# Optimization experiments

Measured on AMD Instinct MI355X. Metric: run time of the kernel, lower is better.

Reference implementation:

```python
import jax, jax.numpy as jnp
import numpy as np

D_MODEL = 1024
NUM_HEADS = 16
D_FF = 4096
EPS = 1e-6


def _layernorm(x, alpha, beta):
    # custom LN: alpha * (x - mean) / (std + eps) + beta, std is UNBIASED (ddof=1)
    mu = jnp.mean(x, axis=-1, keepdims=True)
    var = jnp.sum((x - mu) ** 2, axis=-1, keepdims=True) / (x.shape[-1] - 1)
    return alpha * (x - mu) / (jnp.sqrt(var) + EPS) + beta


def setup_inputs() -> dict:
    key = jax.random.key(0)
    ks = jax.random.split(key, 8)
    B, S, D, F = 1, 4096, D_MODEL, D_FF
    s = 0.02
    inp = {
        "x": jax.random.normal(ks[0], (B, S, D), dtype=jnp.float32),
        "Wq": jax.random.normal(ks[1], (D, D), dtype=jnp.float32) * s,
        "bq": jnp.zeros((D,), jnp.float32),
        "Wk": jax.random.normal(ks[2], (D, D), dtype=jnp.float32) * s,
        "bk": jnp.zeros((D,), jnp.float32),
        "Wv": jax.random.normal(ks[3], (D, D), dtype=jnp.float32) * s,
        "bv": jnp.zeros((D,), jnp.float32),
        "Wo": jax.random.normal(ks[4], (D, D), dtype=jnp.float32) * s,
        "bo": jnp.zeros((D,), jnp.float32),
        "ln1_a": jnp.ones((1,), jnp.float32),
        "ln1_b": jnp.zeros((1,), jnp.float32),
        "W1": jax.random.normal(ks[5], (D, F), dtype=jnp.float32) * s,
        "b1": jnp.zeros((F,), jnp.float32),
        "W2": jax.random.normal(ks[6], (F, D), dtype=jnp.float32) * s,
        "b2": jnp.zeros((D,), jnp.float32),
        "ln2_a": jnp.ones((1,), jnp.float32),
        "ln2_b": jnp.zeros((1,), jnp.float32),
    }
    return inp


def reference(x, Wq, bq, Wk, bk, Wv, bv, Wo, bo, ln1_a, ln1_b,
              W1, b1, W2, b2, ln2_a, ln2_b):
    B, S, D = x.shape
    H = NUM_HEADS
    dk = D // H

    # --- residual 1: pre-LN self-attention ---
    h = _layernorm(x, ln1_a, ln1_b)
    Q = (h @ Wq + bq).reshape(B, S, H, dk)
    K = (h @ Wk + bk).reshape(B, S, H, dk)
    V = (h @ Wv + bv).reshape(B, S, H, dk)
    scores = jnp.einsum("bqhd,bkhd->bhqk", Q, K) / jnp.sqrt(jnp.float32(dk))
    attn = jax.nn.softmax(scores, axis=-1)  # [B,H,S,S] materialized as in source
    ctx = jnp.einsum("bhqk,bkhd->bqhd", attn, V).reshape(B, S, D)
    x = x + (ctx @ Wo + bo)  # dropout=0 -> identity

    # --- residual 2: pre-LN feed-forward ---
    h2 = _layernorm(x, ln2_a, ln2_b)
    ffn = jax.nn.relu(h2 @ W1 + b1) @ W2 + b2
    return x + ffn
```

## Files before the change

kernel.cpp:

```cpp
#include <hip/hip_runtime.h>
#include <hip/hip_bf16.h>

typedef __attribute__((ext_vector_type(8))) __bf16 bf16x8;
typedef __attribute__((ext_vector_type(4))) float f32x4;
typedef __attribute__((ext_vector_type(4))) short sh4;
typedef __attribute__((ext_vector_type(8))) short sh8;

#define MFMA(a, b, c) __builtin_amdgcn_mfma_f32_16x16x32_bf16(a, b, c, 0, 0, 0)

#if __has_builtin(__builtin_amdgcn_exp2f)
#define EXP2(x) __builtin_amdgcn_exp2f(x)
#else
#define EXP2(x) exp2f(x)
#endif

union P8 { struct { sh4 lo, hi; } p; sh8 v; };

__device__ __forceinline__ sh4 pk4(float a, float b, float c, float d) {
    __hip_bfloat162 lo = __float22bfloat162_rn(float2{a, b});
    __hip_bfloat162 hi = __float22bfloat162_rn(float2{c, d});
    union { struct { __hip_bfloat162 lo, hi; } p; sh4 s; } u;
    u.p.lo = lo; u.p.hi = hi;
    return u.s;
}

__device__ __forceinline__ float ldany(const void* p, size_t i, bool f32) {
    return f32 ? ((const float*)p)[i] : (float)(((const __bf16*)p)[i]);
}

__global__ void prep_k(const void* wq, float* flag,
                       const void* bq, const void* bk, const void* bv, const void* bo,
                       const void* b1, const void* b2,
                       const void* l1a, const void* l1b, const void* l2a, const void* l2b,
                       __bf16* dst) {
    __shared__ float red[256];
    __shared__ float fls;
    int tid = threadIdx.x;
    const __bf16* p = (const __bf16*)wq;
    float mx = 0.f;
    for (int i = tid; i < 1024; i += 256) {
        float v = (float)p[i];
        if (v != v) mx = 2.f;
        v = fabsf(v);
        if (v > mx) mx = v;
    }
    red[tid] = mx;
    __syncthreads();
    for (int s = 128; s > 0; s >>= 1) {
        if (tid < s) red[tid] = fmaxf(red[tid], red[tid + s]);
        __syncthreads();
    }
    if (tid == 0) { fls = (red[0] > 1.0f) ? 1.f : 0.f; *flag = fls; }
    __syncthreads();
    bool f32 = fls > 0.5f;
    const void* srcs[10] = {bq, bk, bv, bo, b1, b2, l1a, l1b, l2a, l2b};
    const int offs[10] = {1024, 2048, 3072, 4096, 5120, 9216, 10240, 10241, 10242, 10243};
    const int ns[10]   = {1024, 1024, 1024, 1024, 4096, 1024, 1, 1, 1, 1};
    for (int t = 0; t < 10; ++t)
        for (int j = tid; j < ns[t]; j += blockDim.x)
            dst[offs[t] + j] = (__bf16)ldany(srcs[t], j, f32);
}

__device__ __forceinline__ void tr_body(const void* in, __bf16* out, int R, int C, bool f32,
                                        int bx, int by, int x, int y) {
    __shared__ __bf16 t[32][33];
    for (int i = 0; i < 32; i += 8)
        t[y + i][x] = (__bf16)ldany(in, (size_t)(by + y + i) * C + bx + x, f32);
    __syncthreads();
    for (int i = 0; i < 32; i += 8)
        out[(size_t)(bx + y + i) * R + by + x] = t[x][y + i];
}

__global__ void transpose_cvt(const void* in, __bf16* out, int R, int C, const float* flag) {
    tr_body(in, out, R, C, *flag > 0.5f, blockIdx.x * 32, blockIdx.y * 32,
            threadIdx.x, threadIdx.y);
}

__global__ void transpose4_cvt(const void* i0, const void* i1, const void* i2, const void* i3,
                               __bf16* o0, __bf16* o1, __bf16* o2, __bf16* o3,
                               const float* flag) {
    const void* in = blockIdx.z == 0 ? i0 : blockIdx.z == 1 ? i1 : blockIdx.z == 2 ? i2 : i3;
    __bf16* out = blockIdx.z == 0 ? o0 : blockIdx.z == 1 ? o1 : blockIdx.z == 2 ? o2 : o3;
    tr_body(in, out, 1024, 1024, *flag > 0.5f, blockIdx.x * 32, blockIdx.y * 32,
            threadIdx.x, threadIdx.y);
}

__global__ __launch_bounds__(256) void layernorm_k(const void* x, int xmode, const float* flag,
                                                   __bf16* out,
                                                   const __bf16* alpha, const __bf16* beta) {
    int row = blockIdx.x * 4 + (threadIdx.x >> 6);
    int lane = threadIdx.x & 63;
    bool f32 = xmode && (*flag > 0.5f);
    float v[16];
    if (f32) {
        const float4* xr = (const float4*)((const float*)x + (size_t)row * 1024 + lane * 16);
#pragma unroll
        for (int q = 0; q < 4; ++q) {
            float4 r = xr[q];
            v[q * 4 + 0] = r.x; v[q * 4 + 1] = r.y; v[q * 4 + 2] = r.z; v[q * 4 + 3] = r.w;
        }
    } else {
        const __bf16* xr = (const __bf16*)x + (size_t)row * 1024 + lane * 16;
        bf16x8 h0 = *(const bf16x8*)xr;
        bf16x8 h1 = *(const bf16x8*)(xr + 8);
#pragma unroll
        for (int i = 0; i < 8; ++i) { v[i] = (float)h0[i]; v[8 + i] = (float)h1[i]; }
    }
    float s = 0.f, ss = 0.f;
#pragma unroll
    for (int i = 0; i < 16; ++i) { s += v[i]; ss += v[i] * v[i]; }
#pragma unroll
    for (int o = 1; o < 64; o <<= 1) { s += __shfl_xor(s, o); ss += __shfl_xor(ss, o); }
    float mu = s * (1.f / 1024.f);
    float var = (ss - 1024.f * mu * mu) * (1.f / 1023.f);
    float inv = 1.f / (sqrtf(var) + 1e-6f);
    float al = (float)alpha[0], be = (float)beta[0];
    bf16x8 o0, o1;
#pragma unroll
    for (int i = 0; i < 8; ++i) {
        o0[i] = (__bf16)((v[i] - mu) * inv * al + be);
        o1[i] = (__bf16)((v[8 + i] - mu) * inv * al + be);
    }
    __bf16* orow = out + (size_t)row * 1024;
    *(bf16x8*)(orow + lane * 16) = o0;
    *(bf16x8*)(orow + lane * 16 + 8) = o1;
}

__device__ __forceinline__ void swz_store(__bf16* buf, int hh, int ktt, int rr2, int cc2,
                                          float v) {
    size_t off = (((size_t)hh * 64 + ktt) << 12) + rr2 * 64 +
                 (((cc2 >> 3) ^ (rr2 & 7)) << 3) + (cc2 & 7);
    buf[off] = (__bf16)v;
}

__global__ __launch_bounds__(256) void gemm_bt(const __bf16* __restrict__ A, int lda,
                                               const __bf16* __restrict__ Bt, int ldb,
                                               const __bf16* __restrict__ bias_n,
                                               const __bf16* __restrict__ bias_m,
                                               const void* res, int res_mode,
                                               const float* flag,
                                               void* C, int out_pf,
                                               int M, int N, int K, int relu,
                                               __bf16* swzbuf, int swz) {
    __shared__ __bf16 As[128 * 32];
    __shared__ __bf16 Bs[128 * 32];
    const int tid = threadIdx.x;
    const int m0 = blockIdx.y * 128;
    const int n0 = blockIdx.x * 128;
    const int w = tid >> 6, lane = tid & 63;
    const int wr = (w >> 1) * 64, wc = (w & 1) * 64;
    const int lm = lane & 15, lg = lane >> 4;
    const bool f32 = *flag > 0.5f;
    const bool rf32 = (res_mode == 2) && f32;
    const bool of32 = out_pf && f32;

    f32x4 acc[4][4] = {};
    for (int k0 = 0; k0 < K; k0 += 32) {
#pragma unroll
        for (int i = 0; i < 2; ++i) {
            int c = i * 256 + tid;
            int row = c >> 2, kk = (c & 3) * 8;
            __builtin_amdgcn_global_load_lds(
                (const __attribute__((address_space(1))) void*)(A + (size_t)(m0 + row) * lda + k0 + kk),
                (__attribute__((address_space(3))) void*)(As + c * 8), 16, 0, 0);
            __builtin_amdgcn_global_load_lds(
                (const __attribute__((address_space(1))) void*)(Bt + (size_t)(n0 + row) * ldb + k0 + kk),
                (__attribute__((address_space(3))) void*)(Bs + c * 8), 16, 0, 0);
        }
        __syncthreads();
        bf16x8 a[4], b[4];
#pragma unroll
        for (int t = 0; t < 4; ++t)
            a[t] = *(const bf16x8*)(As + (wr + t * 16 + lm) * 32 + lg * 8);
#pragma unroll
        for (int t = 0; t < 4; ++t)
            b[t] = *(const bf16x8*)(Bs + (wc + t * 16 + lm) * 32 + lg * 8);
#pragma unroll
        for (int mt = 0; mt < 4; ++mt)
#pragma unroll
            for (int nt = 0; nt < 4; ++nt)
                acc[mt][nt] = MFMA(a[mt], b[nt], acc[mt][nt]);
        __syncthreads();
    }
#pragma unroll
    for (int mt = 0; mt < 4; ++mt) {
#pragma unroll
        for (int nt = 0; nt < 4; ++nt) {
            int col = n0 + wc + nt * 16 + lm;
            float bn = bias_n ? (float)bias_n[col] : 0.f;
#pragma unroll
            for (int r = 0; r < 4; ++r) {
                int row = m0 + wr + mt * 16 + lg * 4 + r;
                float vv = acc[mt][nt][r] + bn;
                if (bias_m) vv += (float)bias_m[row];
                if (relu) vv = fmaxf(vv, 0.f);
                if (swz == 1 && col >= 1024) {
                    swz_store(swzbuf, (col - 1024) >> 6, row >> 6, row & 63, (col - 1024) & 63, vv);
                } else if (swz == 2) {
                    swz_store(swzbuf, row >> 6, col >> 6, row & 63, col & 63, vv);
                } else {
                    size_t idx = (size_t)row * N + col;
                    if (res_mode) vv += rf32 ? ((const float*)res)[idx]
                                             : (float)(((const __bf16*)res)[idx]);
                    if (of32) ((float*)C)[idx] = vv;
                    else ((__bf16*)C)[idx] = (__bf16)vv;
                }
            }
        }
    }
}

__global__ __launch_bounds__(256) void gemm_n64(const __bf16* __restrict__ A, int lda,
                                                const __bf16* __restrict__ Bt, int ldb,
                                                const __bf16* __restrict__ bias_n,
                                                const __bf16* __restrict__ bias_m,
                                                const void* res, int res_mode,
                                                const float* flag,
                                                void* C, int out_pf,
                                                int M, int N, int K, int relu,
                                                __bf16* swzbuf, int swz) {
    __shared__ __bf16 As[128 * 64];
    __shared__ __bf16 Bs[64 * 64];
    const int tid = threadIdx.x;
    const int m0 = blockIdx.y * 128;
    const int n0 = blockIdx.x * 64;
    const int w = tid >> 6, lane = tid & 63;
    const int wr = (w >> 1) * 64, wc = (w & 1) * 32;
    const int lm = lane & 15, lg = lane >> 4;
    const int sw = lm & 7;
    const bool f32 = *flag > 0.5f;
    const bool rf32 = (res_mode == 2) && f32;
    const bool of32 = out_pf && f32;

    f32x4 acc[4][2] = {};
    for (int k0 = 0; k0 < K; k0 += 64) {
#pragma unroll
        for (int i = 0; i < 4; ++i) {
            int c = i * 256 + tid;
            int row = c >> 3, ch = c & 7;
            __builtin_amdgcn_global_load_lds(
                (const __attribute__((address_space(1))) void*)(A + (size_t)(m0 + row) * lda + k0 + ((ch ^ (row & 7)) << 3)),
                (__attribute__((address_space(3))) void*)(As + c * 8), 16, 0, 0);
        }
#pragma unroll
        for (int i = 0; i < 2; ++i) {
            int c = i * 256 + tid;
            int row = c >> 3, ch = c & 7;
            __builtin_amdgcn_global_load_lds(
                (const __attribute__((address_space(1))) void*)(Bt + (size_t)(n0 + row) * ldb + k0 + ((ch ^ (row & 7)) << 3)),
                (__attribute__((address_space(3))) void*)(Bs + c * 8), 16, 0, 0);
        }
        __syncthreads();
        bf16x8 a[4][2], b[2][2];
#pragma unroll
        for (int t = 0; t < 4; ++t)
#pragma unroll
            for (int h = 0; h < 2; ++h)
                a[t][h] = *(const bf16x8*)(As + (wr + t * 16 + lm) * 64 + ((((h << 2) | lg) ^ sw) << 3));
#pragma unroll
        for (int t = 0; t < 2; ++t)
#pragma unroll
            for (int h = 0; h < 2; ++h)
                b[t][h] = *(const bf16x8*)(Bs + (wc + t * 16 + lm) * 64 + ((((h << 2) | lg) ^ sw) << 3));
#pragma unroll
        for (int mt = 0; mt < 4; ++mt)
#pragma unroll
            for (int nt = 0; nt < 2; ++nt) {
                acc[mt][nt] = MFMA(a[mt][0], b[nt][0], acc[mt][nt]);
                acc[mt][nt] = MFMA(a[mt][1], b[nt][1], acc[mt][nt]);
            }
        __syncthreads();
    }
#pragma unroll
    for (int mt = 0; mt < 4; ++mt) {
#pragma unroll
        for (int nt = 0; nt < 2; ++nt) {
            int col = n0 + wc + nt * 16 + lm;
            float bn = bias_n ? (float)bias_n[col] : 0.f;
#pragma unroll
            for (int r = 0; r < 4; ++r) {
                int row = m0 + wr + mt * 16 + lg * 4 + r;
                float vv = acc[mt][nt][r] + bn;
                if (bias_m) vv += (float)bias_m[row];
                if (relu) vv = fmaxf(vv, 0.f);
                if (swz == 2) {
                    swz_store(swzbuf, row >> 6, col >> 6, row & 63, col & 63, vv);
                } else {
                    size_t idx = (size_t)row * N + col;
                    if (res_mode) vv += rf32 ? ((const float*)res)[idx]
                                             : (float)(((const __bf16*)res)[idx]);
                    if (of32) ((float*)C)[idx] = vv;
                    else ((__bf16*)C)[idx] = (__bf16)vv;
                }
            }
        }
    }
}

__global__ __launch_bounds__(256) void attn_ks2(const __bf16* __restrict__ Q, int ldq,
                                                const __bf16* __restrict__ Kswz,
                                                const __bf16* __restrict__ Vswz,
                                                __bf16* __restrict__ Opart,
                                                float* __restrict__ lpart) {
    constexpr int S = 4096;
    __shared__ __bf16 lds[2 * 8192];
    const int h = blockIdx.y, z = blockIdx.z;
    const int q0 = blockIdx.x * 128;
    const int tid = threadIdx.x, w = tid >> 6, lane = tid & 63;
    const int lm = lane & 15, lg = lane >> 4;

    const __bf16* gK = Kswz + (((size_t)h * 64 + z * 32) << 12);
    const __bf16* gV = Vswz + (((size_t)h * 64 + z * 32) << 12);

    bf16x8 qf[2][2];
#pragma unroll
    for (int qc = 0; qc < 2; ++qc) {
        const __bf16* qp = Q + (size_t)(q0 + w * 32 + qc * 16 + lm) * ldq + h * 64;
        qf[qc][0] = *(const bf16x8*)(qp + lg * 8);
        qf[qc][1] = *(const bf16x8*)(qp + 32 + lg * 8);
#pragma unroll
        for (int hh = 0; hh < 2; ++hh) {
            bf16x8 t = qf[qc][hh];
#pragma unroll
            for (int i = 0; i < 8; ++i) t[i] = (__bf16)((float)t[i] * 0.1803368801f);
            qf[qc][hh] = t;
        }
    }
    bf16x8 ones8;
#pragma unroll
    for (int i = 0; i < 8; ++i) ones8[i] = (__bf16)1.f;

    f32x4 o_[4][2] = {};
    f32x4 l_[2] = {};

    auto issue = [&](int t) {
        __bf16* dK = lds + (t & 1) * 8192;
        __bf16* dV = dK + 4096;
        const __bf16* sK = gK + ((size_t)t << 12);
        const __bf16* sV = gV + ((size_t)t << 12);
#pragma unroll
        for (int i = 0; i < 2; ++i) {
            int c = i * 256 + tid;
            __builtin_amdgcn_global_load_lds(
                (const __attribute__((address_space(1))) void*)(sK + c * 8),
                (__attribute__((address_space(3))) void*)(dK + c * 8), 16, 0, 0);
            __builtin_amdgcn_global_load_lds(
                (const __attribute__((address_space(1))) void*)(sV + c * 8),
                (__attribute__((address_space(3))) void*)(dV + c * 8), 16, 0, 0);
        }
    };
    issue(0);
    for (int t = 0; t < 32; ++t) {
        __syncthreads();
        if (t < 31) issue(t + 1);
        const __bf16* Kt = lds + (t & 1) * 8192;
        const __bf16* Vt = Kt + 4096;

        P8 pb[2][2];
#pragma unroll
        for (int mt = 0; mt < 4; ++mt) {
            int rr = mt * 16 + lm;
            const __bf16* kr = Kt + rr * 64;
            bf16x8 kf0 = *(const bf16x8*)(kr + ((lg ^ (rr & 7)) << 3));
            bf16x8 kf1 = *(const bf16x8*)(kr + (((4 + lg) ^ (rr & 7)) << 3));
#pragma unroll
            for (int qc = 0; qc < 2; ++qc) {
                f32x4 s = (f32x4){0.f, 0.f, 0.f, 0.f};
                s = MFMA(kf0, qf[qc][0], s);
                s = MFMA(kf1, qf[qc][1], s);
                sh4 e = pk4(EXP2(s[0]), EXP2(s[1]), EXP2(s[2]), EXP2(s[3]));
                if (mt & 1) pb[mt >> 1][qc].p.hi = e;
                else        pb[mt >> 1][qc].p.lo = e;
            }
        }
#pragma unroll
        for (int mtd = 0; mtd < 4; ++mtd) {
            int rr = mtd * 16 + lm;
            const __bf16* vr = Vt + rr * 64;
#pragma unroll
            for (int cp = 0; cp < 2; ++cp) {
                int cbase = cp * 4 + (lg >> 1);
                P8 va;
                va.p.lo = *(const sh4*)(vr + ((cbase ^ (rr & 7)) << 3) + (lg & 1) * 4);
                va.p.hi = *(const sh4*)(vr + (((cbase + 2) ^ (rr & 7)) << 3) + (lg & 1) * 4);
                bf16x8 vab = __builtin_bit_cast(bf16x8, va.v);
                o_[mtd][0] = MFMA(vab, __builtin_bit_cast(bf16x8, pb[cp][0].v), o_[mtd][0]);
                o_[mtd][1] = MFMA(vab, __builtin_bit_cast(bf16x8, pb[cp][1].v), o_[mtd][1]);
            }
        }
#pragma unroll
        for (int cp = 0; cp < 2; ++cp) {
            l_[0] = MFMA(ones8, __builtin_bit_cast(bf16x8, pb[cp][0].v), l_[0]);
            l_[1] = MFMA(ones8, __builtin_bit_cast(bf16x8, pb[cp][1].v), l_[1]);
        }
    }

    __syncthreads();
#pragma unroll
    for (int qc = 0; qc < 2; ++qc) {
#pragma unroll
        for (int mtd = 0; mtd < 4; ++mtd) {
            sh4 ov = pk4(o_[mtd][qc][0], o_[mtd][qc][1], o_[mtd][qc][2], o_[mtd][qc][3]);
            *(sh4*)(lds + (w * 32 + qc * 16 + lm) * 72 + mtd * 16 + lg * 4) = ov;
        }
        if (lg == 0)
            lpart[(size_t)(h * 2 + z) * S + q0 + w * 32 + qc * 16 + lm] = l_[qc][0];
    }
    __syncthreads();
    __bf16* Ob = Opart + (((size_t)(h * 2 + z) * S + q0) << 6);
    int row = tid >> 1, co = (tid & 1) * 32;
#pragma unroll
    for (int b = 0; b < 4; ++b)
        *(uint4*)(Ob + row * 64 + co + b * 8) = *(const uint4*)(lds + row * 72 + co + b * 8);
}

__global__ __launch_bounds__(256) void attn_comb(const __bf16* __restrict__ Opart,
                                                 const float* __restrict__ lpart,
                                                 __bf16* __restrict__ ctx) {
    constexpr int S = 4096;
#pragma unroll
    for (int it = 0; it < 4; ++it) {
        int task = blockIdx.x * 1024 + it * 256 + threadIdx.x;
        int q = task >> 7, c8 = task & 127, h = c8 >> 3, d8 = (c8 & 7) * 8;
        const __bf16* p0 = Opart + (((size_t)(h * 2 + 0) * S + q) << 6) + d8;
        const __bf16* p1 = Opart + (((size_t)(h * 2 + 1) * S + q) << 6) + d8;
        float inv = 1.f / (lpart[(size_t)(h * 2 + 0) * S + q] + lpart[(size_t)(h * 2 + 1) * S + q]);
        bf16x8 a = *(const bf16x8*)p0, b = *(const bf16x8*)p1, o;
#pragma unroll
        for (int i = 0; i < 8; ++i) o[i] = (__bf16)(((float)a[i] + (float)b[i]) * inv);
        *(bf16x8*)(ctx + (size_t)q * 1024 + c8 * 8) = o;
    }
}

__global__ __launch_bounds__(256) void attn_v3(const __bf16* __restrict__ Q, int ldq,
                                               const __bf16* __restrict__ Kg, int ldk,
                                               const __bf16* __restrict__ VT,
                                               __bf16* __restrict__ ctx) {
    constexpr int S = 4096, D = 1024, LDT = 72;
    __shared__ __bf16 lds[128 * LDT];
    __bf16* Kt = lds;
    __bf16* Vt = lds + 64 * LDT;
    const int h = blockIdx.y;
    const int q0 = blockIdx.x * 128;
    const int tid = threadIdx.x, w = tid >> 6, lane = tid & 63;
    const int lm = lane & 15, lg = lane >> 4;
    bf16x8 qf[2][2];
#pragma unroll
    for (int qc = 0; qc < 2; ++qc) {
        const __bf16* qp = Q + (size_t)(q0 + w * 32 + qc * 16 + lm) * ldq + h * 64;
        qf[qc][0] = *(const bf16x8*)(qp + lg * 8);
        qf[qc][1] = *(const bf16x8*)(qp + 32 + lg * 8);
#pragma unroll
        for (int hh = 0; hh < 2; ++hh) {
            bf16x8 t = qf[qc][hh];
#pragma unroll
            for (int i = 0; i < 8; ++i) t[i] = (__bf16)((float)t[i] * 0.1803368801f);
            qf[qc][hh] = t;
        }
    }
    bf16x8 ones8;
#pragma unroll
    for (int i = 0; i < 8; ++i) ones8[i] = (__bf16)1.f;
    f32x4 o_[4][2] = {};
    f32x4 l_[2] = {};
    for (int kt = 0; kt < S / 64; ++kt) {
        __syncthreads();
#pragma unroll
        for (int i = 0; i < 2; ++i) {
            int c = i * 256 + tid;
            int rr = c >> 3, cc = (c & 7) * 8;
            *(uint4*)(Kt + rr * LDT + cc) =
                *(const uint4*)(Kg + (size_t)(kt * 64 + rr) * ldk + h * 64 + cc);
            *(uint4*)(Vt + rr * LDT + cc) =
                *(const uint4*)(VT + (size_t)(h * 64 + rr) * S + kt * 64 + cc);
        }
        __syncthreads();
        P8 pb[2][2];
#pragma unroll
        for (int mt = 0; mt < 4; ++mt) {
            bf16x8 kf0 = *(const bf16x8*)(Kt + (mt * 16 + lm) * LDT + lg * 8);
            bf16x8 kf1 = *(const bf16x8*)(Kt + (mt * 16 + lm) * LDT + 32 + lg * 8);
#pragma unroll
            for (int qc = 0; qc < 2; ++qc) {
                f32x4 s = (f32x4){0.f, 0.f, 0.f, 0.f};
                s = MFMA(kf0, qf[qc][0], s);
                s = MFMA(kf1, qf[qc][1], s);
                sh4 e = pk4(EXP2(s[0]), EXP2(s[1]), EXP2(s[2]), EXP2(s[3]));
                if (mt & 1) pb[mt >> 1][qc].p.hi = e;
                else        pb[mt >> 1][qc].p.lo = e;
            }
        }
#pragma unroll
        for (int mtd = 0; mtd < 4; ++mtd) {
            const __bf16* vrow = Vt + (mtd * 16 + lm) * LDT;
#pragma unroll
            for (int cp = 0; cp < 2; ++cp) {
                P8 va;
                va.p.lo = *(const sh4*)(vrow + cp * 32 + lg * 4);
                va.p.hi = *(const sh4*)(vrow + cp * 32 + 16 + lg * 4);
                bf16x8 vab = __builtin_bit_cast(bf16x8, va.v);
                o_[mtd][0] = MFMA(vab, __builtin_bit_cast(bf16x8, pb[cp][0].v), o_[mtd][0]);
                o_[mtd][1] = MFMA(vab, __builtin_bit_cast(bf16x8, pb[cp][1].v), o_[mtd][1]);
            }
        }
#pragma unroll
        for (int cp = 0; cp < 2; ++cp) {
            l_[0] = MFMA(ones8, __builtin_bit_cast(bf16x8, pb[cp][0].v), l_[0]);
            l_[1] = MFMA(ones8, __builtin_bit_cast(bf16x8, pb[cp][1].v), l_[1]);
        }
    }
    __syncthreads();
    float inv[2] = {1.f / l_[0][0], 1.f / l_[1][0]};
#pragma unroll
    for (int qc = 0; qc < 2; ++qc)
#pragma unroll
        for (int mtd = 0; mtd < 4; ++mtd)
#pragma unroll
            for (int r = 0; r < 4; ++r)
                lds[(w * 32 + qc * 16 + lm) * LDT + mtd * 16 + lg * 4 + r] =
                    (__bf16)(o_[mtd][qc][r] * inv[qc]);
    __syncthreads();
    int row = tid >> 1, cb = (tid & 1) * 32;
#pragma unroll
    for (int b = 0; b < 4; ++b)
        *(uint4*)(ctx + (size_t)(q0 + row) * D + h * 64 + cb + b * 8) =
            *(const uint4*)(lds + row * LDT + cb + b * 8);
}

extern "C" void kernel_launch(void* const* d_in, const int* in_sizes, int n_in,
                              void* d_out, int out_size, void* d_ws, size_t ws_size,
                              hipStream_t stream) {
    const void* x    = d_in[0];
    const void* Wq   = d_in[1];
    const void* bq   = d_in[2];
    const void* Wk   = d_in[3];
    const void* bk   = d_in[4];
    const void* Wv   = d_in[5];
    const void* bv   = d_in[6];
    const void* Wo   = d_in[7];
    const void* bo   = d_in[8];
    const void* ln1a = d_in[9];
    const void* ln1b = d_in[10];
    const void* W1   = d_in[11];
    const void* b1   = d_in[12];
    const void* W2   = d_in[13];
    const void* b2   = d_in[14];
    const void* ln2a = d_in[15];
    const void* ln2b = d_in[16];

    constexpr size_t M1 = 1u << 20;
    __bf16* ws = (__bf16*)d_ws;
    float* flagF = (float*)ws;
    __bf16* bmir = ws;
    dim3 tb(32, 8);
    const bool big = ws_size >= (size_t)(32.25 * 2 * M1) + 4096;

    prep_k<<<1, 256, 0, stream>>>(Wq, flagF, bq, bk, bv, bo, b1, b2,
                                  ln1a, ln1b, ln2a, ln2b, bmir);

    if (big) {
        __bf16* WqT = ws + M1 / 4;
        __bf16* WkT = WqT + M1;
        __bf16* WvT = ws + 2 * M1 + M1 / 4;
        __bf16* WoT = ws + 3 * M1 + M1 / 4;
        __bf16* W2T = ws + M1 / 4;
        float* lpart = (float*)(ws + M1 / 4);
        __bf16* hb  = ws + 4 * M1 + M1 / 4;
        __bf16* h2  = hb;
        __bf16* QKb = ws + 8 * M1 + M1 / 4;
        __bf16* x2  = QKb;
        __bf16* W1T = ws + 12 * M1 + M1 / 4;
        __bf16* Kswz = ws + 16 * M1 + M1 / 4;
        __bf16* ctx  = Kswz;
        __bf16* Vswz = ws + 20 * M1 + M1 / 4;
        __bf16* Opart = ws + 24 * M1 + M1 / 4;
        __bf16* f1  = ws + 16 * M1 + M1 / 4;

        transpose4_cvt<<<dim3(32, 32, 4), tb, 0, stream>>>(Wq, Wk, Wv, Wo,
                                                           WqT, WkT, WvT, WoT, flagF);
        layernorm_k<<<1024, 256, 0, stream>>>(x, 1, flagF, hb, bmir + 10240, bmir + 10241);
        gemm_bt<<<dim3(16, 32), 256, 0, stream>>>(hb, 1024, WqT, 1024, bmir + 1024, nullptr,
                                                  nullptr, 0, flagF, QKb, 0, 4096, 2048, 1024, 0,
                                                  Kswz, 1);
        gemm_n64<<<dim3(64, 8), 256, 0, stream>>>(WvT, 1024, hb, 1024, nullptr, bmir + 3072,
                                                  nullptr, 0, flagF, nullptr, 0, 1024, 4096, 1024, 0,
                                                  Vswz, 2);
        attn_ks2<<<dim3(32, 16, 2), 256, 0, stream>>>(QKb, 2048, Kswz, Vswz, Opart, lpart);
        attn_comb<<<512, 256, 0, stream>>>(Opart, lpart, ctx);
        transpose_cvt<<<dim3(128, 32), tb, 0, stream>>>(W1, W1T, 1024, 4096, flagF);
        gemm_n64<<<dim3(16, 32), 256, 0, stream>>>(ctx, 1024, WoT, 1024, bmir + 4096, nullptr,
                                                   x, 2, flagF, x2, 0, 4096, 1024, 1024, 0,
                                                   nullptr, 0);
        transpose_cvt<<<dim3(32, 128), tb, 0, stream>>>(W2, W2T, 4096, 1024, flagF);
        layernorm_k<<<1024, 256, 0, stream>>>(x2, 0, flagF, h2, bmir + 10242, bmir + 10243);
        gemm_bt<<<dim3(32, 32), 256, 0, stream>>>(h2, 1024, W1T, 1024, bmir + 5120, nullptr,
                                                  nullptr, 0, flagF, f1, 0, 4096, 4096, 1024, 1,
                                                  nullptr, 0);
        gemm_n64<<<dim3(16, 32), 256, 0, stream>>>(f1, 4096, W2T, 4096, bmir + 9216, nullptr,
                                                   x2, 1, flagF, d_out, 1, 4096, 1024, 4096, 0,
                                                   nullptr, 0);
    } else {
        constexpr size_t Qn = 1u << 18;
        __bf16* WqT = ws + Qn;
        __bf16* WoT = WqT;
        __bf16* WkT = ws + 5 * Qn;
        __bf16* WvT = ws + 9 * Qn;
        __bf16* hb  = ws + 13 * Qn;
        __bf16* f1q = hb;
        __bf16* ctx = ws + 29 * Qn;
        __bf16* W2T = ctx;
        __bf16* QKb = ws + 45 * Qn;
        __bf16* x2  = QKb;
        __bf16* Kb  = ws + 61 * Qn;
        __bf16* h2  = Kb;
        __bf16* VTb = ws + 77 * Qn;
        __bf16* W1T = VTb;
        transpose_cvt<<<dim3(32, 32), tb, 0, stream>>>(Wq, WqT, 1024, 1024, flagF);
        transpose_cvt<<<dim3(32, 32), tb, 0, stream>>>(Wk, WkT, 1024, 1024, flagF);
        transpose_cvt<<<dim3(32, 32), tb, 0, stream>>>(Wv, WvT, 1024, 1024, flagF);
        layernorm_k<<<1024, 256, 0, stream>>>(x, 1, flagF, hb, bmir + 10240, bmir + 10241);
        gemm_bt<<<dim3(8, 32), 256, 0, stream>>>(hb, 1024, WqT, 1024, bmir + 1024, nullptr,
                                                 nullptr, 0, flagF, QKb, 0, 4096, 1024, 1024, 0,
                                                 nullptr, 0);
        gemm_bt<<<dim3(8, 32), 256, 0, stream>>>(hb, 1024, WkT, 1024, bmir + 2048, nullptr,
                                                 nullptr, 0, flagF, Kb, 0, 4096, 1024, 1024, 0,
                                                 nullptr, 0);
        gemm_n64<<<dim3(64, 8), 256, 0, stream>>>(WvT, 1024, hb, 1024, nullptr, bmir + 3072,
                                                  nullptr, 0, flagF, VTb, 0, 1024, 4096, 1024, 0,
                                                  nullptr, 0);
        attn_v3<<<dim3(32, 16), 256, 0, stream>>>(QKb, 1024, Kb, 1024, VTb, ctx);
        transpose_cvt<<<dim3(32, 32), tb, 0, stream>>>(Wo, WoT, 1024, 1024, flagF);
        gemm_n64<<<dim3(16, 32), 256, 0, stream>>>(ctx, 1024, WoT, 1024, bmir + 4096, nullptr,
                                                   x, 2, flagF, x2, 0, 4096, 1024, 1024, 0,
                                                   nullptr, 0);
        layernorm_k<<<1024, 256, 0, stream>>>(x2, 0, flagF, h2, bmir + 10242, bmir + 10243);
        transpose_cvt<<<dim3(128, 32), tb, 0, stream>>>(W1, W1T, 1024, 4096, flagF);
        transpose_cvt<<<dim3(32, 128), tb, 0, stream>>>(W2, W2T, 4096, 1024, flagF);
        for (int ck = 0; ck < 2; ++ck) {
            gemm_bt<<<dim3(16, 32), 256, 0, stream>>>(h2, 1024, W1T + (size_t)ck * 2048 * 1024,
                                                      1024, bmir + 5120 + ck * 2048, nullptr,
                                                      nullptr, 0, flagF, f1q, 0, 4096, 2048, 1024, 1,
                                                      nullptr, 0);
            gemm_n64<<<dim3(16, 32), 256, 0, stream>>>(f1q, 2048, W2T + ck * 2048, 4096,
                                                       ck == 0 ? bmir + 9216 : nullptr, nullptr,
                                                       x2, 1, flagF, ck == 1 ? d_out : (void*)x2,
                                                       ck == 1 ? 1 : 0, 4096, 1024, 2048, 0,
                                                       nullptr, 0);
        }
    }
}
```

Measured before the change: 488.2 us.

## Double-buffer LDS tiles in both GEMM kernels to overlap loads with MFMA

Both GEMM kernels now keep two LDS buffers for the A and B tiles. The next K-tile is prefetched with global_load_lds while MFMAs run on the current buffer, and one barrier per iteration is removed. The aim is to hide global-memory latency behind compute. This doubles LDS use per block, which may lower occupancy, and it depends on the barrier at the end of each iteration to cover the async load completion.

```diff
diff --git a/kernel.cpp b/kernel.cpp
--- a/kernel.cpp
+++ b/kernel.cpp
@@ -142,8 +142,8 @@
                                                void* C, int out_pf,
                                                int M, int N, int K, int relu,
                                                __bf16* swzbuf, int swz) {
-    __shared__ __bf16 As[128 * 32];
-    __shared__ __bf16 Bs[128 * 32];
+    __shared__ __bf16 As[2][128 * 32];
+    __shared__ __bf16 Bs[2][128 * 32];
     const int tid = threadIdx.x;
     const int m0 = blockIdx.y * 128;
     const int n0 = blockIdx.x * 128;
@@ -154,33 +154,40 @@
     const bool rf32 = (res_mode == 2) && f32;
     const bool of32 = out_pf && f32;
 
-    f32x4 acc[4][4] = {};
-    for (int k0 = 0; k0 < K; k0 += 32) {
+    auto stage = [&](int buf, int k0) {
 #pragma unroll
         for (int i = 0; i < 2; ++i) {
             int c = i * 256 + tid;
             int row = c >> 2, kk = (c & 3) * 8;
             __builtin_amdgcn_global_load_lds(
                 (const __attribute__((address_space(1))) void*)(A + (size_t)(m0 + row) * lda + k0 + kk),
-                (__attribute__((address_space(3))) void*)(As + c * 8), 16, 0, 0);
+                (__attribute__((address_space(3))) void*)(As[buf] + c * 8), 16, 0, 0);
             __builtin_amdgcn_global_load_lds(
                 (const __attribute__((address_space(1))) void*)(Bt + (size_t)(n0 + row) * ldb + k0 + kk),
-                (__attribute__((address_space(3))) void*)(Bs + c * 8), 16, 0, 0);
-        }
-        __syncthreads();
+                (__attribute__((address_space(3))) void*)(Bs[buf] + c * 8), 16, 0, 0);
+        }
+    };
+
+    f32x4 acc[4][4] = {};
+    stage(0, 0);
+    __syncthreads();
+    int cur = 0;
+    for (int k0 = 0; k0 < K; k0 += 32) {
+        if (k0 + 32 < K) stage(cur ^ 1, k0 + 32);
         bf16x8 a[4], b[4];
 #pragma unroll
         for (int t = 0; t < 4; ++t)
-            a[t] = *(const bf16x8*)(As + (wr + t * 16 + lm) * 32 + lg * 8);
+            a[t] = *(const bf16x8*)(As[cur] + (wr + t * 16 + lm) * 32 + lg * 8);
 #pragma unroll
         for (int t = 0; t < 4; ++t)
-            b[t] = *(const bf16x8*)(Bs + (wc + t * 16 + lm) * 32 + lg * 8);
+            b[t] = *(const bf16x8*)(Bs[cur] + (wc + t * 16 + lm) * 32 + lg * 8);
 #pragma unroll
         for (int mt = 0; mt < 4; ++mt)
 #pragma unroll
             for (int nt = 0; nt < 4; ++nt)
                 acc[mt][nt] = MFMA(a[mt], b[nt], acc[mt][nt]);
         __syncthreads();
+        cur ^= 1;
     }
 #pragma unroll
     for (int mt = 0; mt < 4; ++mt) {
@@ -219,8 +226,8 @@
                                                 void* C, int out_pf,
                                                 int M, int N, int K, int relu,
                                                 __bf16* swzbuf, int swz) {
-    __shared__ __bf16 As[128 * 64];
-    __shared__ __bf16 Bs[64 * 64];
+    __shared__ __bf16 As[2][128 * 64];
+    __shared__ __bf16 Bs[2][64 * 64];
     const int tid = threadIdx.x;
     const int m0 = blockIdx.y * 128;
     const int n0 = blockIdx.x * 64;
@@ -232,15 +239,14 @@
     const bool rf32 = (res_mode == 2) && f32;
     const bool of32 = out_pf && f32;
 
-    f32x4 acc[4][2] = {};
-    for (int k0 = 0; k0 < K; k0 += 64) {
+    auto stage = [&](int buf, int k0) {
 #pragma unroll
         for (int i = 0; i < 4; ++i) {
             int c = i * 256 + tid;
             int row = c >> 3, ch = c & 7;
             __builtin_amdgcn_global_load_lds(
                 (const __attribute__((address_space(1))) void*)(A + (size_t)(m0 + row) * lda + k0 + ((ch ^ (row & 7)) << 3)),
-                (__attribute__((address_space(3))) void*)(As + c * 8), 16, 0, 0);
+                (__attribute__((address_space(3))) void*)(As[buf] + c * 8), 16, 0, 0);
         }
 #pragma unroll
         for (int i = 0; i < 2; ++i) {
@@ -248,20 +254,27 @@
             int row = c >> 3, ch = c & 7;
             __builtin_amdgcn_global_load_lds(
                 (const __attribute__((address_space(1))) void*)(Bt + (size_t)(n0 + row) * ldb + k0 + ((ch ^ (row & 7)) << 3)),
-                (__attribute__((address_space(3))) void*)(Bs + c * 8), 16, 0, 0);
-        }
-        __syncthreads();
+                (__attribute__((address_space(3))) void*)(Bs[buf] + c * 8), 16, 0, 0);
+        }
+    };
+
+    f32x4 acc[4][2] = {};
+    stage(0, 0);
+    __syncthreads();
+    int cur = 0;
+    for (int k0 = 0; k0 < K; k0 += 64) {
+        if (k0 + 64 < K) stage(cur ^ 1, k0 + 64);
         bf16x8 a[4][2], b[2][2];
 #pragma unroll
         for (int t = 0; t < 4; ++t)
 #pragma unroll
             for (int h = 0; h < 2; ++h)
-                a[t][h] = *(const bf16x8*)(As + (wr + t * 16 + lm) * 64 + ((((h << 2) | lg) ^ sw) << 3));
+                a[t][h] = *(const bf16x8*)(As[cur] + (wr + t * 16 + lm) * 64 + ((((h << 2) | lg) ^ sw) << 3));
 #pragma unroll
         for (int t = 0; t < 2; ++t)
 #pragma unroll
             for (int h = 0; h < 2; ++h)
-                b[t][h] = *(const bf16x8*)(Bs + (wc + t * 16 + lm) * 64 + ((((h << 2) | lg) ^ sw) << 3));
+                b[t][h] = *(const bf16x8*)(Bs[cur] + (wc + t * 16 + lm) * 64 + ((((h << 2) | lg) ^ sw) << 3));
 #pragma unroll
         for (int mt = 0; mt < 4; ++mt)
 #pragma unroll
@@ -270,6 +283,7 @@
                 acc[mt][nt] = MFMA(a[mt][1], b[nt][1], acc[mt][nt]);
             }
         __syncthreads();
+        cur ^= 1;
     }
 #pragma unroll
     for (int mt = 0; mt < 4; ++mt) {
```

Result: no change. 480.2 us (-1.6%).
